# Performance work log

Measured on AMD Instinct MI355X. Metric: run time of the kernel, lower is better.

## Reference

```python
import jax, jax.numpy as jnp
import numpy as np
from functools import partial
from jax import lax

B, K, CLIP_DIM, SBERT_DIM, D_MODEL, R_RANK, ATTN_DIM, PMAX = 128, 1024, 768, 384, 256, 64, 256, 8
RHO = 0.35

def _normalize(x, axis=-1, eps=1e-12):
    return x / jnp.maximum(jnp.linalg.norm(x, axis=axis, keepdims=True), eps)

def _build_graph():
    rng = np.random.default_rng(0)
    pid = np.zeros((K, PMAX), np.int32)
    pm = np.zeros((K, PMAX), bool)
    for i in range(K - 1):  # node i's parents are in (i, K); root = K-1 has none
        n = int(rng.integers(1, PMAX + 1))
        n = min(n, K - 1 - i)
        cands = rng.choice(np.arange(i + 1, K), size=n, replace=False)
        pid[i, :n] = cands
        pm[i, :n] = True
    order = np.arange(K - 1, -1, -1, dtype=np.int32)  # parents before children
    return jnp.asarray(pid), jnp.asarray(pm), jnp.asarray(order)

def setup_inputs() -> dict:
    key = jax.random.key(0)
    ks = iter(jax.random.split(key, 32))
    r = lambda shape, s=0.02: jax.random.normal(next(ks), shape, jnp.float32) * s
    pid, pm, order = _build_graph()
    return {
        "t_clip": jax.random.normal(next(ks), (B, CLIP_DIM), jnp.float32),
        "v_clip": jax.random.normal(next(ks), (B, CLIP_DIM), jnp.float32),
        "concept_sbert": jax.random.normal(next(ks), (K, SBERT_DIM), jnp.float32),
        "Wt": r((CLIP_DIM, D_MODEL)), "bt": jnp.zeros((D_MODEL,)),
        "Wv": r((CLIP_DIM, D_MODEL)), "bv": jnp.zeros((D_MODEL,)),
        "Wc": r((SBERT_DIM, D_MODEL)), "bc": jnp.zeros((D_MODEL,)),
        "Wp1": r((3 * D_MODEL, 2 * D_MODEL)), "bp1": jnp.zeros((2 * D_MODEL,)),
        "Wp2": r((2 * D_MODEL, D_MODEL)), "bp2": jnp.zeros((D_MODEL,)),
        "Wm1": r((3 * D_MODEL, 2 * D_MODEL)), "bm1": jnp.zeros((2 * D_MODEL,)),
        "Wm2": r((2 * D_MODEL, D_MODEL)), "bm2": jnp.zeros((D_MODEL,)),
        "tau_logits": jnp.zeros((K,)),
        "U": r((D_MODEL, R_RANK)), "V": r((D_MODEL, R_RANK)),
        "Wg1": r((SBERT_DIM, R_RANK)), "bg1": jnp.zeros((R_RANK,)),
        "Wg2": r((R_RANK, R_RANK)), "bg2": jnp.zeros((R_RANK,)),
        "w_out": r((K, R_RANK)), "b_out": jnp.zeros((K,)),
        "concept_q": r((K, ATTN_DIM)),
        "parents_idx": pid, "parents_mask": pm, "order": order,
    }

def _forward(t_clip, v_clip, concept_sbert, Wt, bt, Wv, bv, Wc, bc,
             Wp1, bp1, Wp2, bp2, Wm1, bm1, Wm2, bm2, tau_logits,
             U, V, Wg1, bg1, Wg2, bg2, w_out, b_out, concept_q,
             parents_idx, parents_mask, order):
    gelu = partial(jax.nn.gelu, approximate=False)  # torch nn.GELU default = exact erf
    t = _normalize(t_clip) @ Wt + bt                 # [B, D]
    v = _normalize(v_clip) @ Wv + bv                 # [B, D]
    d = concept_sbert @ Wc + bc                      # [K, D]
    # x = [v, t, d] broadcast to [B, K, 3D]
    x = jnp.concatenate([
        jnp.broadcast_to(v[:, None, :], (t.shape[0], K, D_MODEL)),
        jnp.broadcast_to(t[:, None, :], (t.shape[0], K, D_MODEL)),
        jnp.broadcast_to(d[None, :, :], (t.shape[0], K, D_MODEL)),
    ], axis=-1)
    h_plus = gelu(x @ Wp1 + bp1) @ Wp2 + bp2
    h_minus = gelu(x @ Wm1 + bm1) @ Wm2 + bm2
    tau = jax.nn.sigmoid(tau_logits)[None, :, None]
    h = tau * h_plus + (1.0 - tau) * h_minus         # [B, K, D]
    u = jnp.einsum('bkd,dr->bkr', h, U)
    vv = jnp.einsum('bkd,dr->bkr', h, V)
    g = gelu(concept_sbert @ Wg1 + bg1) @ Wg2 + bg2  # [K, R]
    inter = u * vv * g[None, :, :]
    logits = jnp.einsum('bkr,kr->bk', inter, w_out) + b_out[None, :]
    p = jax.nn.sigmoid(logits)                        # [B, K]
    # --- top-down hierarchical attention + multiplicative aggregation ---
    q = _normalize(concept_q)                         # [K, A]
    def step(p_hat, node):
        par = parents_idx[node]                       # [P] int
        m = parents_mask[node]                        # [P] bool
        scores = jnp.where(m, q[par] @ q[node], -1e9)
        alpha = jax.nn.softmax(scores)                # [P]
        vals = p_hat[:, par]                          # [B, P] gather of parent probs
        prod = jnp.prod(jnp.where(m[None, :], alpha[None, :] * vals, 1.0), axis=-1)
        new = jnp.where(m.any(), RHO * p[:, node] + (1.0 - RHO) * prod, p_hat[:, node])
        return p_hat.at[:, node].set(new), None       # scatter write
    p_hat, _ = lax.scan(step, p, order)
    return p_hat

def reference(t_clip, v_clip, concept_sbert, Wt, bt, Wv, bv, Wc, bc,
              Wp1, bp1, Wp2, bp2, Wm1, bm1, Wm2, bm2, tau_logits,
              U, V, Wg1, bg1, Wg2, bg2, w_out, b_out, concept_q,
              parents_idx, parents_mask, order):
    return _forward(t_clip, v_clip, concept_sbert, Wt, bt, Wv, bv, Wc, bc,
                    Wp1, bp1, Wp2, bp2, Wm1, bm1, Wm2, bm2, tau_logits,
                    U, V, Wg1, bg1, Wg2, bg2, w_out, b_out, concept_q,
                    parents_idx, parents_mask, order)
```

## Files before the change

kernel.cpp:

```cpp
#include <hip/hip_runtime.h>
#include <math.h>

typedef __attribute__((ext_vector_type(8))) short short8;
typedef __attribute__((ext_vector_type(4))) float float4v;
typedef __attribute__((ext_vector_type(2))) float float2v;

struct P {
  const float *t_clip, *v_clip, *sbert;
  const float *Wt, *bt, *Wv, *bv, *Wc, *bc;
  const float *Wp1, *bp1, *Wp2, *bp2, *Wm1, *bm1, *Wm2, *bm2;
  const float *tau_logits, *U, *V, *Wg1, *bg1, *Wg2, *bg2, *w_out, *b_out, *concept_q;
  const int *pid;
  float *Ap, *Am;
  unsigned short *Ctp, *Ctm;
  unsigned short *Wpk, *Wmk;
  float *biasPM, *tau, *gw, *aprod;
  unsigned short *parS;
  int *sorted, *lvlStart, *nlev;
  float *pOut;
};

__device__ __forceinline__ unsigned short bf16ru(float f) {
    unsigned u = __float_as_uint(f);
    u += 0x7fffu + ((u >> 16) & 1u);
    return (unsigned short)(u >> 16);
}

__device__ __forceinline__ unsigned packpair(float2v a, unsigned c) {
    float2v cb;
    cb.x = __uint_as_float(c << 16);
    cb.y = __uint_as_float(c & 0xffff0000u);
    float2v x = a + cb;
    float2v t = x * x;
    float2v i = t * (-0.06649038f) + 0.39894228f;
    float2v p = x * i + 0.5f;
    float2v g = x * p;
    union { float2v f; unsigned u[2]; } gu; gu.f = g;
    return __builtin_amdgcn_perm(gu.u[1], gu.u[0], 0x07060302u);
}


__device__ void ab_f(const P& a, int b, float* smemF) {
    float* raw = smemF;
    float* vt  = smemF + 1536;
    float* red = smemF + 2060;
    int t = threadIdx.x;
    float sT = 0.f, sV = 0.f;
    for (int i = t; i < 768; i += 256) {
        float xt = a.t_clip[(size_t)b * 768 + i];
        float xv = a.v_clip[(size_t)b * 768 + i];
        raw[i] = xt; raw[768 + i] = xv;
        sT = fmaf(xt, xt, sT); sV = fmaf(xv, xv, sV);
    }
    for (int mk = 32; mk; mk >>= 1) { sT += __shfl_xor(sT, mk); sV += __shfl_xor(sV, mk); }
    if ((t & 63) == 0) { red[t >> 6] = sT; red[4 + (t >> 6)] = sV; }
    __syncthreads();
    float scT = 1.0f / fmaxf(sqrtf(red[0] + red[1] + red[2] + red[3]), 1e-12f);
    float scV = 1.0f / fmaxf(sqrtf(red[4] + red[5] + red[6] + red[7]), 1e-12f);
    float accT = 0.f, accV = 0.f;
    for (int d = 0; d < 768; ++d) {
        accT = fmaf(raw[d],       a.Wt[(size_t)d * 256 + t], accT);
        accV = fmaf(raw[768 + d], a.Wv[(size_t)d * 256 + t], accV);
    }
    vt[t]       = accV * scV + a.bv[t];
    vt[256 + t] = accT * scT + a.bt[t];
    __syncthreads();
    int mat = t >> 7, j0 = (t & 127) * 4;
    const float* W1 = mat ? a.Wm1 : a.Wp1;
    const float* b1 = mat ? a.bm1 : a.bp1;
    float* out = mat ? a.Am : a.Ap;
    float a0 = 0, a1 = 0, a2 = 0, a3 = 0;
    for (int d = 0; d < 512; ++d) {
        float4 w = *(const float4*)&W1[(size_t)d * 512 + j0];
        float x = vt[d];
        a0 = fmaf(x, w.x, a0); a1 = fmaf(x, w.y, a1);
        a2 = fmaf(x, w.z, a2); a3 = fmaf(x, w.w, a3);
    }
    float4 bb = *(const float4*)&b1[j0];
    float4 o; o.x = a0 + bb.x; o.y = a1 + bb.y; o.z = a2 + bb.z; o.w = a3 + bb.w;
    *(float4*)&out[(size_t)b * 512 + j0] = o;
}

__device__ void c_f(const P& a, int blk, float* smemF) {
    int k0 = blk * 2;
    float* sb = smemF;
    float* dr = smemF + 768;
    int t = threadIdx.x;
    for (int i = t; i < 768; i += 256) sb[i] = a.sbert[(size_t)k0 * 384 + i];
    __syncthreads();
    float d0 = 0.f, d1 = 0.f;
    for (int dd = 0; dd < 384; ++dd) {
        float w = a.Wc[(size_t)dd * 256 + t];
        d0 = fmaf(sb[dd], w, d0);
        d1 = fmaf(sb[384 + dd], w, d1);
    }
    dr[t] = d0 + a.bc[t];
    dr[256 + t] = d1 + a.bc[t];
    __syncthreads();
    int mat = t >> 7, j0 = (t & 127) * 4;
    const float* W1 = mat ? a.Wm1 : a.Wp1;
    unsigned short* out = mat ? a.Ctm : a.Ctp;
    float a00 = 0, a01 = 0, a02 = 0, a03 = 0, a10 = 0, a11 = 0, a12 = 0, a13 = 0;
    for (int dd = 0; dd < 256; ++dd) {
        float4 w = *(const float4*)&W1[(size_t)(512 + dd) * 512 + j0];
        float x0 = dr[dd], x1 = dr[256 + dd];
        a00 = fmaf(x0, w.x, a00); a01 = fmaf(x0, w.y, a01);
        a02 = fmaf(x0, w.z, a02); a03 = fmaf(x0, w.w, a03);
        a10 = fmaf(x1, w.x, a10); a11 = fmaf(x1, w.y, a11);
        a12 = fmaf(x1, w.z, a12); a13 = fmaf(x1, w.w, a13);
    }
    int step = j0 >> 5, quad = (j0 >> 3) & 3, e0 = j0 & 7;
#pragma unroll
    for (int r = 0; r < 2; ++r) {
        int k = k0 + r;
        size_t idx = (size_t)(k >> 4) * 8192 + step * 512 + quad * 128 + (k & 15) * 8 + e0;
        ushort4 o;
        o.x = bf16ru(r ? a10 : a00); o.y = bf16ru(r ? a11 : a01);
        o.z = bf16ru(r ? a12 : a02); o.w = bf16ru(r ? a13 : a03);
        *(ushort4*)&out[idx] = o;
    }
}

__device__ void packW_f(const float* __restrict__ W2, const float* __restrict__ U,
                        const float* __restrict__ V, unsigned short* __restrict__ outP, int rel) {
    int idx = rel * 256 + threadIdx.x;
    int j = idx >> 7, c = idx & 127;
    const float* uv = (c < 64) ? (U + c) : (V + (c - 64));
    float acc = 0.f;
    for (int d = 0; d < 256; ++d) acc = fmaf(W2[(size_t)j * 256 + d], uv[(size_t)d * 64], acc);
    size_t o = (size_t)(j >> 5) * 4096 + (c >> 4) * 512 + ((j >> 3) & 3) * 128 + (c & 15) * 8 + (j & 7);
    outP[o] = bf16ru(acc);
}

__device__ void gw_f(const P& a, int blk, float* ghid) {
    int t = threadIdx.x, wv = t >> 6, lane = t & 63;
    int k = blk * 4 + wv;
    float acc = a.bg1[lane];
    for (int d = 0; d < 384; ++d)
        acc = fmaf(a.sbert[(size_t)k * 384 + d], a.Wg1[(size_t)d * 64 + lane], acc);
    ghid[wv * 64 + lane] = 0.5f * acc * (1.0f + erff(acc * 0.7071067811865475f));
    __syncthreads();
    float acc2 = a.bg2[lane];
    for (int d = 0; d < 64; ++d)
        acc2 = fmaf(ghid[wv * 64 + d], a.Wg2[(size_t)d * 64 + lane], acc2);
    a.gw[(size_t)k * 64 + lane] = acc2 * a.w_out[(size_t)k * 64 + lane];
}

__device__ void alpha_f(const P& a, int blk) {
    int t = threadIdx.x, wv = t >> 6, lane = t & 63;
    int node = blk * 4 + wv;
    int slot = lane >> 3, e = lane & 7;
    int par = a.pid[node * 8 + slot];
    const float4* qk = (const float4*)(a.concept_q + (size_t)node * 256);
    const float4* qp = (const float4*)(a.concept_q + (size_t)par * 256);
    float dq = 0, np = 0, ns = 0;
#pragma unroll
    for (int i = 0; i < 8; ++i) {
        float4 x = qp[e * 8 + i], y = qk[e * 8 + i];
        dq += x.x * y.x + x.y * y.y + x.z * y.z + x.w * y.w;
        np += x.x * x.x + x.y * x.y + x.z * x.z + x.w * x.w;
        ns += y.x * y.x + y.y * y.y + y.z * y.z + y.w * y.w;
    }
#pragma unroll
    for (int mk = 1; mk <= 4; mk <<= 1) {
        dq += __shfl_xor(dq, mk); np += __shfl_xor(np, mk); ns += __shfl_xor(ns, mk);
    }
    float score = dq / fmaxf(sqrtf(np) * sqrtf(ns), 1e-24f);
    float sc[8]; int pv[8];
#pragma unroll
    for (int s = 0; s < 8; ++s) { sc[s] = __shfl(score, s * 8); pv[s] = __shfl(par, s * 8); }
    float mx = -1e30f;
#pragma unroll
    for (int s = 0; s < 8; ++s) if (pv[s] != 0) mx = fmaxf(mx, sc[s]);
    float sum = 0.f;
#pragma unroll
    for (int s = 0; s < 8; ++s) sum += (pv[s] != 0) ? expf(sc[s] - mx) : 0.0f;
    float ap = 1.0f;
#pragma unroll
    for (int s = 0; s < 8; ++s) if (pv[s] != 0) ap *= expf(sc[s] - mx) / sum;
    if (lane == 0) a.aprod[node] = ap;
    if (e == 0) a.parS[node * 8 + slot] = (par != 0) ? (unsigned short)par : (unsigned short)1024;
}

__device__ void misc_f(const P& a, int g) {
    int t = threadIdx.x;
    if (g == 0) {
        int c = t & 127;
        const float* bb = (t < 128) ? a.bp2 : a.bm2;
        const float* uv = (c < 64) ? (a.U + c) : (a.V + (c - 64));
        float acc = 0.f;
        for (int d = 0; d < 256; ++d) acc = fmaf(bb[d], uv[(size_t)d * 64], acc);
        a.biasPM[t] = acc;
    } else {
        int k = (g - 1) * 256 + t;
        a.tau[k] = 1.0f / (1.0f + expf(-a.tau_logits[k]));
    }
}

__device__ void levels_f(const P& a, int* smemI) {
    volatile int* lvl = smemI;
    int* cnt  = smemI + 1024;
    int* ofs  = smemI + 2048;
    int* ping = smemI + 3072;
    int* pong = smemI + 3328;
    int* mflag = smemI + 3584;
    int t = threadIdx.x;
    int par[4][8]; int hasm[4];
#pragma unroll
    for (int r = 0; r < 4; ++r) {
        int n = t * 4 + r, h = 0;
#pragma unroll
        for (int s = 0; s < 8; ++s) { int p = a.pid[n * 8 + s]; par[r][s] = p; h |= (p != 0); }
        hasm[r] = h; lvl[n] = 0;
    }
    if (t == 0) mflag[1] = 0;
    __syncthreads();
    for (int round = 0; round < 200; ++round) {
        if (t == 0) mflag[0] = 0;
        __syncthreads();
        int ch = 0;
        for (int sub = 0; sub < 8; ++sub) {
#pragma unroll
            for (int r = 0; r < 4; ++r) {
                if (!hasm[r]) continue;
                int mx = 0;
#pragma unroll
                for (int s = 0; s < 8; ++s) { int p = par[r][s]; if (p) mx = max(mx, lvl[p]); }
                int nl = mx + 1;
                if (nl > lvl[t * 4 + r]) { lvl[t * 4 + r] = nl; ch = 1; }
            }
        }
        if (ch) mflag[0] = 1;
        __syncthreads();
        if (mflag[0] == 0) break;
    }
    int lm = 0;
    for (int r = 0; r < 4; ++r) lm = max(lm, lvl[t * 4 + r]);
    atomicMax(&mflag[1], lm);
    for (int r = 0; r < 4; ++r) cnt[t * 4 + r] = 0;
    __syncthreads();
    for (int r = 0; r < 4; ++r) atomicAdd(&cnt[lvl[t * 4 + r]], 1);
    __syncthreads();
    int c0 = cnt[t * 4], c1 = cnt[t * 4 + 1], c2 = cnt[t * 4 + 2], c3 = cnt[t * 4 + 3];
    ping[t] = c0 + c1 + c2 + c3;
    __syncthreads();
    int* src = ping; int* dst = pong;
    for (int off = 1; off < 256; off <<= 1) {
        int v = src[t];
        if (t >= off) v += src[t - off];
        dst[t] = v;
        __syncthreads();
        int* tmp = src; src = dst; dst = tmp;
    }
    int excl = (t == 0) ? 0 : src[t - 1];
    ofs[t * 4] = excl; ofs[t * 4 + 1] = excl + c0;
    ofs[t * 4 + 2] = excl + c0 + c1; ofs[t * 4 + 3] = excl + c0 + c1 + c2;
#pragma unroll
    for (int r = 0; r < 4; ++r) a.lvlStart[t * 4 + r] = ofs[t * 4 + r];
    if (t == 0) { a.lvlStart[1024] = 1024; a.nlev[0] = mflag[1] + 1; }
    __syncthreads();
    for (int r = 0; r < 4; ++r) {
        int n = t * 4 + r;
        int pos = atomicAdd(&ofs[lvl[n]], 1);
        a.sorted[pos] = n;
    }
}

__global__ void __launch_bounds__(256) prep_kernel(P a) {
    __shared__ float smemF[4096];
    int bid = blockIdx.x;
    if (bid == 0) { levels_f(a, (int*)smemF); return; }
    bid -= 1;
    if (bid < 128) { ab_f(a, bid, smemF); return; }
    bid -= 128;
    if (bid < 512) { c_f(a, bid, smemF); return; }
    bid -= 512;
    if (bid < 256) { packW_f(a.Wp2, a.U, a.V, a.Wpk, bid); return; }
    bid -= 256;
    if (bid < 256) { packW_f(a.Wm2, a.U, a.V, a.Wmk, bid); return; }
    bid -= 256;
    if (bid < 256) { gw_f(a, bid, smemF); return; }
    bid -= 256;
    if (bid < 256) { alpha_f(a, bid); return; }
    bid -= 256;
    misc_f(a, bid);
}

__global__ void __launch_bounds__(256, 2) main_kernel(P a) {
    __shared__ float apL[4 * 512];
    __shared__ char wbuf[2][16384];
    int tid = threadIdx.x;
    int wv = tid >> 6, lane = tid & 63;
    int b0 = (blockIdx.x >> 4) * 2;
    int k0 = (blockIdx.x & 15) << 6;
    int m = lane & 15, quad = lane >> 4;

    for (int i = tid; i < 512; i += 256) {
        int arr = i >> 7, off = i & 127;
        const float* src = (arr == 0) ? (a.Ap + (size_t)b0 * 512)
                         : (arr == 1) ? (a.Ap + (size_t)(b0 + 1) * 512)
                         : (arr == 2) ? (a.Am + (size_t)b0 * 512)
                                      : (a.Am + (size_t)(b0 + 1) * 512);
        ((float4v*)apL)[i] = ((const float4v*)src)[off];
    }

    const char* wpG = (const char*)a.Wpk;
    const char* wmG = (const char*)a.Wmk;
    int so = tid * 16;
    uint4 wreg[4];
#define LOADW(step) do { \
    wreg[0] = *(const uint4*)(wpG + (size_t)(step) * 8192 + so); \
    wreg[1] = *(const uint4*)(wpG + (size_t)(step) * 8192 + 4096 + so); \
    wreg[2] = *(const uint4*)(wmG + (size_t)(step) * 8192 + so); \
    wreg[3] = *(const uint4*)(wmG + (size_t)(step) * 8192 + 4096 + so); } while (0)
#define WRITEW(buf) do { \
    *(uint4*)(&wbuf[buf][so])         = wreg[0]; \
    *(uint4*)(&wbuf[buf][4096 + so])  = wreg[1]; \
    *(uint4*)(&wbuf[buf][8192 + so])  = wreg[2]; \
    *(uint4*)(&wbuf[buf][12288 + so]) = wreg[3]; } while (0)

    int kt = (k0 >> 4) + wv;
    const char* cpB = (const char*)a.Ctp + (size_t)kt * 16384 + quad * 256 + m * 16;
    const char* cmB = (const char*)a.Ctm + (size_t)kt * 16384 + quad * 256 + m * 16;

    float4v accP[2][8], accM[2][8];
#pragma unroll
    for (int b = 0; b < 2; ++b)
#pragma unroll
        for (int i = 0; i < 8; ++i) { accP[b][i] = (float4v)0.0f; accM[b][i] = (float4v)0.0f; }

    LOADW(0);
    WRITEW(0);
    uint4 cprN = *(const uint4*)(cpB);
    uint4 cmrN = *(const uint4*)(cmB);
    LOADW(1);
    __syncthreads();

    for (int n = 0; n < 16; ++n) {
        if (n < 15) WRITEW((n + 1) & 1);
        if (n < 14) LOADW(n + 2);
        uint4 cprC = cprN, cmrC = cmrN;
        if (n < 15) {
            cprN = *(const uint4*)(cpB + (n + 1) * 1024);
            cmrN = *(const uint4*)(cmB + (n + 1) * 1024);
        }
        const float* aBase = apL + n * 32 + quad * 8;
        union { uint4 u; short8 s; } fp[2], fm[2];
#pragma unroll
        for (int b = 0; b < 2; ++b) {
            float4v x0 = *(const float4v*)(aBase + b * 512);
            float4v x1 = *(const float4v*)(aBase + b * 512 + 4);
            float4v y0 = *(const float4v*)(aBase + (2 + b) * 512);
            float4v y1 = *(const float4v*)(aBase + (2 + b) * 512 + 4);
            float2v v;
            v.x = x0[0]; v.y = x0[1]; fp[b].u.x = packpair(v, cprC.x);
            v.x = x0[2]; v.y = x0[3]; fp[b].u.y = packpair(v, cprC.y);
            v.x = x1[0]; v.y = x1[1]; fp[b].u.z = packpair(v, cprC.z);
            v.x = x1[2]; v.y = x1[3]; fp[b].u.w = packpair(v, cprC.w);
            v.x = y0[0]; v.y = y0[1]; fm[b].u.x = packpair(v, cmrC.x);
            v.x = y0[2]; v.y = y0[3]; fm[b].u.y = packpair(v, cmrC.y);
            v.x = y1[0]; v.y = y1[1]; fm[b].u.z = packpair(v, cmrC.z);
            v.x = y1[2]; v.y = y1[3]; fm[b].u.w = packpair(v, cmrC.w);
        }
        const char* wB = &wbuf[n & 1][0] + quad * 256 + m * 16;
#pragma unroll
        for (int nt = 0; nt < 8; ++nt) {
            short8 wpf = *(const short8*)(wB + nt * 1024);
            short8 wmf = *(const short8*)(wB + 8192 + nt * 1024);
            accP[0][nt] = __builtin_amdgcn_mfma_f32_16x16x32_bf16(fp[0].s, wpf, accP[0][nt], 0, 0, 0);
            accP[1][nt] = __builtin_amdgcn_mfma_f32_16x16x32_bf16(fp[1].s, wpf, accP[1][nt], 0, 0, 0);
            accM[0][nt] = __builtin_amdgcn_mfma_f32_16x16x32_bf16(fm[0].s, wmf, accM[0][nt], 0, 0, 0);
            accM[1][nt] = __builtin_amdgcn_mfma_f32_16x16x32_bf16(fm[1].s, wmf, accM[1][nt], 0, 0, 0);
        }
        __syncthreads();
    }
#undef LOADW
#undef WRITEW
    int kk[4]; float tv[4];
#pragma unroll
    for (int r = 0; r < 4; ++r) { kk[r] = k0 + wv * 16 + quad * 4 + r; tv[r] = a.tau[kk[r]]; }
    float lsum[2][4] = {{0.f,0.f,0.f,0.f},{0.f,0.f,0.f,0.f}};
#pragma unroll
    for (int t4 = 0; t4 < 4; ++t4) {
        int cU = t4 * 16 + m, cV = cU + 64;
        float bPu = a.biasPM[cU], bMu = a.biasPM[128 + cU];
        float bPv = a.biasPM[cV], bMv = a.biasPM[128 + cV];
#pragma unroll
        for (int r = 0; r < 4; ++r) {
            float g = a.gw[(size_t)kk[r] * 64 + cU];
#pragma unroll
            for (int b = 0; b < 2; ++b) {
                float u  = tv[r] * (accP[b][t4][r] + bPu)     + (1.0f - tv[r]) * (accM[b][t4][r] + bMu);
                float vx = tv[r] * (accP[b][t4 + 4][r] + bPv) + (1.0f - tv[r]) * (accM[b][t4 + 4][r] + bMv);
                lsum[b][r] = fmaf(u * vx, g, lsum[b][r]);
            }
        }
    }
#pragma unroll
    for (int r = 0; r < 4; ++r)
#pragma unroll
        for (int b = 0; b < 2; ++b) {
            float s = lsum[b][r];
            s += __shfl_xor(s, 1); s += __shfl_xor(s, 2); s += __shfl_xor(s, 4); s += __shfl_xor(s, 8);
            if (m == 0) {
                float logit = s + a.b_out[kk[r]];
                a.pOut[(size_t)(b0 + b) * 1024 + kk[r]] = 1.0f / (1.0f + expf(-logit));
            }
        }
}

#define PH_STRIDE 1056
__global__ void __launch_bounds__(256) scan_kernel(P a) {
    __shared__ float ph[4 * PH_STRIDE];
    __shared__ float aprodL[1024];
    __shared__ unsigned short parL[8192];
    __shared__ short sortedL[1024];
    __shared__ int lvlStartL[1025];
    int t = threadIdx.x;
    int b0 = blockIdx.x * 4;
    for (int i = t; i < 1024; i += 256) {
        ((uint4*)parL)[i & 1023] = ((const uint4*)a.parS)[i];
    }
    for (int i = t; i < 1024; i += 256) {
        aprodL[i] = a.aprod[i];
        sortedL[i] = (short)a.sorted[i];
        lvlStartL[i] = a.lvlStart[i];
    }
    if (t == 0) lvlStartL[1024] = 1024;
    for (int i = t; i < 4096; i += 256) {
        int bb = i >> 10, k = i & 1023;
        ph[bb * PH_STRIDE + k] = a.pOut[(size_t)(b0 + bb) * 1024 + k];
    }
    if (t < 4) ph[t * PH_STRIDE + 1024] = 1.0f;
    __syncthreads();
    int nlev = a.nlev[0];
    int w = t >> 6, lane = t & 63;
    float* myph = ph + w * PH_STRIDE;
    for (int L = 1; L < nlev; ++L) {
        int s0 = lvlStartL[L], s1 = lvlStartL[L + 1];
        for (int i = s0 + lane; i < s1; i += 64) {
            int node = sortedL[i];
            ushort4 pA = *(const ushort4*)&parL[node * 8];
            ushort4 pB = *(const ushort4*)&parL[node * 8 + 4];
            float prod = aprodL[node];
            prod *= myph[pA.x] * myph[pA.y];
            prod *= myph[pA.z] * myph[pA.w];
            prod *= myph[pB.x] * myph[pB.y];
            prod *= myph[pB.z] * myph[pB.w];
            myph[node] = fmaf(0.35f, myph[node], 0.65f * prod);
        }
    }
    __syncthreads();
    for (int i = t; i < 4096; i += 256) {
        int bb = i >> 10, k = i & 1023;
        a.pOut[(size_t)(b0 + bb) * 1024 + k] = ph[bb * PH_STRIDE + k];
    }
}

extern "C" void kernel_launch(void* const* d_in, const int* in_sizes, int n_in,
                              void* d_out, int out_size, void* d_ws, size_t ws_size,
                              hipStream_t stream) {
    P a;
    a.t_clip = (const float*)d_in[0];
    a.v_clip = (const float*)d_in[1];
    a.sbert  = (const float*)d_in[2];
    a.Wt  = (const float*)d_in[3];  a.bt  = (const float*)d_in[4];
    a.Wv  = (const float*)d_in[5];  a.bv  = (const float*)d_in[6];
    a.Wc  = (const float*)d_in[7];  a.bc  = (const float*)d_in[8];
    a.Wp1 = (const float*)d_in[9];  a.bp1 = (const float*)d_in[10];
    a.Wp2 = (const float*)d_in[11]; a.bp2 = (const float*)d_in[12];
    a.Wm1 = (const float*)d_in[13]; a.bm1 = (const float*)d_in[14];
    a.Wm2 = (const float*)d_in[15]; a.bm2 = (const float*)d_in[16];
    a.tau_logits = (const float*)d_in[17];
    a.U   = (const float*)d_in[18]; a.V   = (const float*)d_in[19];
    a.Wg1 = (const float*)d_in[20]; a.bg1 = (const float*)d_in[21];
    a.Wg2 = (const float*)d_in[22]; a.bg2 = (const float*)d_in[23];
    a.w_out = (const float*)d_in[24]; a.b_out = (const float*)d_in[25];
    a.concept_q = (const float*)d_in[26];
    a.pid = (const int*)d_in[27];

    char* w = (char*)d_ws;
    a.Ap     = (float*)(w + 0);
    a.Am     = (float*)(w + 262144);
    a.Ctp    = (unsigned short*)(w + 524288);
    a.Ctm    = (unsigned short*)(w + 1572864);
    a.Wpk    = (unsigned short*)(w + 2621440);
    a.Wmk    = (unsigned short*)(w + 2752512);
    a.biasPM = (float*)(w + 2883584);
    a.tau    = (float*)(w + 2884608);
    a.gw     = (float*)(w + 2888704);
    a.parS   = (unsigned short*)(w + 3150848);
    a.aprod  = (float*)(w + 3167232);
    a.sorted = (int*)(w + 3171328);
    a.lvlStart = (int*)(w + 3175424);
    a.nlev     = (int*)(w + 3179648);
    a.pOut = (float*)d_out;

    prep_kernel<<<1670, 256, 0, stream>>>(a);
    main_kernel<<<1024, 256, 0, stream>>>(a);
    scan_kernel<<<32, 256, 0, stream>>>(a);
}
```

Measured before the change: 282.6 us.

## Split prep into cache-warming and compute kernels, retile main GEMM per matrix

```diff
diff --git a/kernel.cpp b/kernel.cpp
--- a/kernel.cpp
+++ b/kernel.cpp
@@ -17,6 +17,7 @@
   float *biasPM, *tau, *gw, *aprod;
   unsigned short *parS;
   int *sorted, *lvlStart, *nlev;
+  float *sink;
   float *pOut;
 };
 
@@ -40,85 +41,13 @@
 }
 
 
-__device__ void ab_f(const P& a, int b, float* smemF) {
-    float* raw = smemF;
-    float* vt  = smemF + 1536;
-    float* red = smemF + 2060;
-    int t = threadIdx.x;
-    float sT = 0.f, sV = 0.f;
-    for (int i = t; i < 768; i += 256) {
-        float xt = a.t_clip[(size_t)b * 768 + i];
-        float xv = a.v_clip[(size_t)b * 768 + i];
-        raw[i] = xt; raw[768 + i] = xv;
-        sT = fmaf(xt, xt, sT); sV = fmaf(xv, xv, sV);
-    }
-    for (int mk = 32; mk; mk >>= 1) { sT += __shfl_xor(sT, mk); sV += __shfl_xor(sV, mk); }
-    if ((t & 63) == 0) { red[t >> 6] = sT; red[4 + (t >> 6)] = sV; }
-    __syncthreads();
-    float scT = 1.0f / fmaxf(sqrtf(red[0] + red[1] + red[2] + red[3]), 1e-12f);
-    float scV = 1.0f / fmaxf(sqrtf(red[4] + red[5] + red[6] + red[7]), 1e-12f);
-    float accT = 0.f, accV = 0.f;
-    for (int d = 0; d < 768; ++d) {
-        accT = fmaf(raw[d],       a.Wt[(size_t)d * 256 + t], accT);
-        accV = fmaf(raw[768 + d], a.Wv[(size_t)d * 256 + t], accV);
-    }
-    vt[t]       = accV * scV + a.bv[t];
-    vt[256 + t] = accT * scT + a.bt[t];
-    __syncthreads();
-    int mat = t >> 7, j0 = (t & 127) * 4;
-    const float* W1 = mat ? a.Wm1 : a.Wp1;
-    const float* b1 = mat ? a.bm1 : a.bp1;
-    float* out = mat ? a.Am : a.Ap;
-    float a0 = 0, a1 = 0, a2 = 0, a3 = 0;
-    for (int d = 0; d < 512; ++d) {
-        float4 w = *(const float4*)&W1[(size_t)d * 512 + j0];
-        float x = vt[d];
-        a0 = fmaf(x, w.x, a0); a1 = fmaf(x, w.y, a1);
-        a2 = fmaf(x, w.z, a2); a3 = fmaf(x, w.w, a3);
-    }
-    float4 bb = *(const float4*)&b1[j0];
-    float4 o; o.x = a0 + bb.x; o.y = a1 + bb.y; o.z = a2 + bb.z; o.w = a3 + bb.w;
-    *(float4*)&out[(size_t)b * 512 + j0] = o;
-}
-
-__device__ void c_f(const P& a, int blk, float* smemF) {
-    int k0 = blk * 2;
-    float* sb = smemF;
-    float* dr = smemF + 768;
-    int t = threadIdx.x;
-    for (int i = t; i < 768; i += 256) sb[i] = a.sbert[(size_t)k0 * 384 + i];
-    __syncthreads();
-    float d0 = 0.f, d1 = 0.f;
-    for (int dd = 0; dd < 384; ++dd) {
-        float w = a.Wc[(size_t)dd * 256 + t];
-        d0 = fmaf(sb[dd], w, d0);
-        d1 = fmaf(sb[384 + dd], w, d1);
-    }
-    dr[t] = d0 + a.bc[t];
-    dr[256 + t] = d1 + a.bc[t];
-    __syncthreads();
-    int mat = t >> 7, j0 = (t & 127) * 4;
-    const float* W1 = mat ? a.Wm1 : a.Wp1;
-    unsigned short* out = mat ? a.Ctm : a.Ctp;
-    float a00 = 0, a01 = 0, a02 = 0, a03 = 0, a10 = 0, a11 = 0, a12 = 0, a13 = 0;
-    for (int dd = 0; dd < 256; ++dd) {
-        float4 w = *(const float4*)&W1[(size_t)(512 + dd) * 512 + j0];
-        float x0 = dr[dd], x1 = dr[256 + dd];
-        a00 = fmaf(x0, w.x, a00); a01 = fmaf(x0, w.y, a01);
-        a02 = fmaf(x0, w.z, a02); a03 = fmaf(x0, w.w, a03);
-        a10 = fmaf(x1, w.x, a10); a11 = fmaf(x1, w.y, a11);
-        a12 = fmaf(x1, w.z, a12); a13 = fmaf(x1, w.w, a13);
-    }
-    int step = j0 >> 5, quad = (j0 >> 3) & 3, e0 = j0 & 7;
-#pragma unroll
-    for (int r = 0; r < 2; ++r) {
-        int k = k0 + r;
-        size_t idx = (size_t)(k >> 4) * 8192 + step * 512 + quad * 128 + (k & 15) * 8 + e0;
-        ushort4 o;
-        o.x = bf16ru(r ? a10 : a00); o.y = bf16ru(r ? a11 : a01);
-        o.z = bf16ru(r ? a12 : a02); o.w = bf16ru(r ? a13 : a03);
-        *(ushort4*)&out[idx] = o;
-    }
+__device__ void warm_f(const float* p, int n4, int blk, float* sink) {
+    float4 s = {0.f, 0.f, 0.f, 0.f};
+    for (int i = blk * 1024 + threadIdx.x; i < n4; i += 1024) {
+        float4 v = ((const float4*)p)[i];
+        s.x += v.x; s.y += v.y; s.z += v.z; s.w += v.w;
+    }
+    if (s.x + s.y + s.z + s.w == 1.234567e37f) *sink = s.x;
 }
 
 __device__ void packW_f(const float* __restrict__ W2, const float* __restrict__ U,
@@ -130,56 +59,6 @@
     for (int d = 0; d < 256; ++d) acc = fmaf(W2[(size_t)j * 256 + d], uv[(size_t)d * 64], acc);
     size_t o = (size_t)(j >> 5) * 4096 + (c >> 4) * 512 + ((j >> 3) & 3) * 128 + (c & 15) * 8 + (j & 7);
     outP[o] = bf16ru(acc);
-}
-
-__device__ void gw_f(const P& a, int blk, float* ghid) {
-    int t = threadIdx.x, wv = t >> 6, lane = t & 63;
-    int k = blk * 4 + wv;
-    float acc = a.bg1[lane];
-    for (int d = 0; d < 384; ++d)
-        acc = fmaf(a.sbert[(size_t)k * 384 + d], a.Wg1[(size_t)d * 64 + lane], acc);
-    ghid[wv * 64 + lane] = 0.5f * acc * (1.0f + erff(acc * 0.7071067811865475f));
-    __syncthreads();
-    float acc2 = a.bg2[lane];
-    for (int d = 0; d < 64; ++d)
-        acc2 = fmaf(ghid[wv * 64 + d], a.Wg2[(size_t)d * 64 + lane], acc2);
-    a.gw[(size_t)k * 64 + lane] = acc2 * a.w_out[(size_t)k * 64 + lane];
-}
-
-__device__ void alpha_f(const P& a, int blk) {
-    int t = threadIdx.x, wv = t >> 6, lane = t & 63;
-    int node = blk * 4 + wv;
-    int slot = lane >> 3, e = lane & 7;
-    int par = a.pid[node * 8 + slot];
-    const float4* qk = (const float4*)(a.concept_q + (size_t)node * 256);
-    const float4* qp = (const float4*)(a.concept_q + (size_t)par * 256);
-    float dq = 0, np = 0, ns = 0;
-#pragma unroll
-    for (int i = 0; i < 8; ++i) {
-        float4 x = qp[e * 8 + i], y = qk[e * 8 + i];
-        dq += x.x * y.x + x.y * y.y + x.z * y.z + x.w * y.w;
-        np += x.x * x.x + x.y * x.y + x.z * x.z + x.w * x.w;
-        ns += y.x * y.x + y.y * y.y + y.z * y.z + y.w * y.w;
-    }
-#pragma unroll
-    for (int mk = 1; mk <= 4; mk <<= 1) {
-        dq += __shfl_xor(dq, mk); np += __shfl_xor(np, mk); ns += __shfl_xor(ns, mk);
-    }
-    float score = dq / fmaxf(sqrtf(np) * sqrtf(ns), 1e-24f);
-    float sc[8]; int pv[8];
-#pragma unroll
-    for (int s = 0; s < 8; ++s) { sc[s] = __shfl(score, s * 8); pv[s] = __shfl(par, s * 8); }
-    float mx = -1e30f;
-#pragma unroll
-    for (int s = 0; s < 8; ++s) if (pv[s] != 0) mx = fmaxf(mx, sc[s]);
-    float sum = 0.f;
-#pragma unroll
-    for (int s = 0; s < 8; ++s) sum += (pv[s] != 0) ? expf(sc[s] - mx) : 0.0f;
-    float ap = 1.0f;
-#pragma unroll
-    for (int s = 0; s < 8; ++s) if (pv[s] != 0) ap *= expf(sc[s] - mx) / sum;
-    if (lane == 0) a.aprod[node] = ap;
-    if (e == 0) a.parS[node * 8 + slot] = (par != 0) ? (unsigned short)par : (unsigned short)1024;
 }
 
 __device__ void misc_f(const P& a, int g) {
@@ -266,147 +145,291 @@
     }
 }
 
-__global__ void __launch_bounds__(256) prep_kernel(P a) {
-    __shared__ float smemF[4096];
+__global__ void __launch_bounds__(256) k0_kernel(P a) {
+    __shared__ int smemI[3600];
     int bid = blockIdx.x;
-    if (bid == 0) { levels_f(a, (int*)smemF); return; }
+    if (bid == 0) { levels_f(a, smemI); return; }
     bid -= 1;
-    if (bid < 128) { ab_f(a, bid, smemF); return; }
-    bid -= 128;
-    if (bid < 512) { c_f(a, bid, smemF); return; }
-    bid -= 512;
     if (bid < 256) { packW_f(a.Wp2, a.U, a.V, a.Wpk, bid); return; }
     bid -= 256;
     if (bid < 256) { packW_f(a.Wm2, a.U, a.V, a.Wmk, bid); return; }
     bid -= 256;
+    if (bid < 5) { misc_f(a, bid); return; }
+    bid -= 5;
+    if (bid < 96) { warm_f(a.Wp1, 98304, bid, a.sink); return; }
+    bid -= 96;
+    if (bid < 96) { warm_f(a.Wm1, 98304, bid, a.sink); return; }
+    bid -= 96;
+    if (bid < 48) { warm_f(a.Wt, 49152, bid, a.sink); return; }
+    bid -= 48;
+    if (bid < 48) { warm_f(a.Wv, 49152, bid, a.sink); return; }
+    bid -= 48;
+    if (bid < 24) { warm_f(a.Wc, 24576, bid, a.sink); return; }
+    bid -= 24;
+    if (bid < 96) { warm_f(a.sbert, 98304, bid, a.sink); return; }
+    bid -= 96;
+    if (bid < 24) { warm_f(a.t_clip, 24576, bid, a.sink); return; }
+    bid -= 24;
+    if (bid < 24) { warm_f(a.v_clip, 24576, bid, a.sink); return; }
+    bid -= 24;
+    if (bid < 64) { warm_f(a.concept_q, 65536, bid, a.sink); return; }
+    bid -= 64;
+    if (bid < 16) { warm_f(a.w_out, 16384, bid, a.sink); return; }
+    bid -= 16;
+    warm_f(a.Wg1, 6144, bid, a.sink);
+}
+
+
+__device__ void ab_f(const P& a, int b, float* smemF) {
+    float* raw = smemF;
+    float* vt  = smemF + 1536;
+    float* red = smemF + 2060;
+    int t = threadIdx.x;
+    float sT = 0.f, sV = 0.f;
+    for (int i = t; i < 768; i += 256) {
+        float xt = a.t_clip[(size_t)b * 768 + i];
+        float xv = a.v_clip[(size_t)b * 768 + i];
+        raw[i] = xt; raw[768 + i] = xv;
+        sT = fmaf(xt, xt, sT); sV = fmaf(xv, xv, sV);
+    }
+    for (int mk = 32; mk; mk >>= 1) { sT += __shfl_xor(sT, mk); sV += __shfl_xor(sV, mk); }
+    if ((t & 63) == 0) { red[t >> 6] = sT; red[4 + (t >> 6)] = sV; }
+    __syncthreads();
+    float scT = 1.0f / fmaxf(sqrtf(red[0] + red[1] + red[2] + red[3]), 1e-12f);
+    float scV = 1.0f / fmaxf(sqrtf(red[4] + red[5] + red[6] + red[7]), 1e-12f);
+    float accT = 0.f, accV = 0.f;
+    for (int d = 0; d < 768; ++d) {
+        accT = fmaf(raw[d],       a.Wt[(size_t)d * 256 + t], accT);
+        accV = fmaf(raw[768 + d], a.Wv[(size_t)d * 256 + t], accV);
+    }
+    vt[t]       = accV * scV + a.bv[t];
+    vt[256 + t] = accT * scT + a.bt[t];
+    __syncthreads();
+    int mat = t >> 7, j0 = (t & 127) * 4;
+    const float* W1 = mat ? a.Wm1 : a.Wp1;
+    const float* b1 = mat ? a.bm1 : a.bp1;
+    float* out = mat ? a.Am : a.Ap;
+    float a0 = 0, a1 = 0, a2 = 0, a3 = 0;
+    for (int d = 0; d < 512; ++d) {
+        float4 w = *(const float4*)&W1[(size_t)d * 512 + j0];
+        float x = vt[d];
+        a0 = fmaf(x, w.x, a0); a1 = fmaf(x, w.y, a1);
+        a2 = fmaf(x, w.z, a2); a3 = fmaf(x, w.w, a3);
+    }
+    float4 bb = *(const float4*)&b1[j0];
+    float4 o; o.x = a0 + bb.x; o.y = a1 + bb.y; o.z = a2 + bb.z; o.w = a3 + bb.w;
+    *(float4*)&out[(size_t)b * 512 + j0] = o;
+}
+
+__device__ void c_f(const P& a, int blk, float* smemF) {
+    int k0 = blk * 4;
+    float* sb = smemF;
+    float* dr = smemF + 1536;
+    int t = threadIdx.x;
+    for (int i = t; i < 1536; i += 256) sb[i] = a.sbert[(size_t)k0 * 384 + i];
+    __syncthreads();
+    float d0 = 0, d1 = 0, d2 = 0, d3 = 0;
+    for (int dd = 0; dd < 384; ++dd) {
+        float w = a.Wc[(size_t)dd * 256 + t];
+        d0 = fmaf(sb[dd], w, d0);
+        d1 = fmaf(sb[384 + dd], w, d1);
+        d2 = fmaf(sb[768 + dd], w, d2);
+        d3 = fmaf(sb[1152 + dd], w, d3);
+    }
+    float bcv = a.bc[t];
+    dr[t] = d0 + bcv; dr[256 + t] = d1 + bcv; dr[512 + t] = d2 + bcv; dr[768 + t] = d3 + bcv;
+    __syncthreads();
+    int mat = t >> 7, j0 = (t & 127) * 4;
+    const float* W1 = mat ? a.Wm1 : a.Wp1;
+    unsigned short* out = mat ? a.Ctm : a.Ctp;
+    float acc[4][4] = {};
+    for (int dd = 0; dd < 256; ++dd) {
+        float4 w = *(const float4*)&W1[(size_t)(512 + dd) * 512 + j0];
+#pragma unroll
+        for (int r = 0; r < 4; ++r) {
+            float x = dr[r * 256 + dd];
+            acc[r][0] = fmaf(x, w.x, acc[r][0]); acc[r][1] = fmaf(x, w.y, acc[r][1]);
+            acc[r][2] = fmaf(x, w.z, acc[r][2]); acc[r][3] = fmaf(x, w.w, acc[r][3]);
+        }
+    }
+    int step = j0 >> 5, quad = (j0 >> 3) & 3, e0 = j0 & 7;
+#pragma unroll
+    for (int r = 0; r < 4; ++r) {
+        int k = k0 + r;
+        size_t idx = (size_t)(k >> 4) * 8192 + step * 512 + quad * 128 + (k & 15) * 8 + e0;
+        ushort4 o;
+        o.x = bf16ru(acc[r][0]); o.y = bf16ru(acc[r][1]);
+        o.z = bf16ru(acc[r][2]); o.w = bf16ru(acc[r][3]);
+        *(ushort4*)&out[idx] = o;
+    }
+}
+
+__device__ void gw_f(const P& a, int blk, float* ghid) {
+    int t = threadIdx.x, wv = t >> 6, lane = t & 63;
+    int k = blk * 4 + wv;
+    float acc = a.bg1[lane];
+    for (int d = 0; d < 384; ++d)
+        acc = fmaf(a.sbert[(size_t)k * 384 + d], a.Wg1[(size_t)d * 64 + lane], acc);
+    ghid[wv * 64 + lane] = 0.5f * acc * (1.0f + erff(acc * 0.7071067811865475f));
+    __syncthreads();
+    float acc2 = a.bg2[lane];
+    for (int d = 0; d < 64; ++d)
+        acc2 = fmaf(ghid[wv * 64 + d], a.Wg2[(size_t)d * 64 + lane], acc2);
+    a.gw[(size_t)k * 64 + lane] = acc2 * a.w_out[(size_t)k * 64 + lane];
+}
+
+__device__ void alpha_f(const P& a, int blk) {
+    int t = threadIdx.x, wv = t >> 6, lane = t & 63;
+    int node = blk * 4 + wv;
+    int slot = lane >> 3, e = lane & 7;
+    int par = a.pid[node * 8 + slot];
+    const float4* qk = (const float4*)(a.concept_q + (size_t)node * 256);
+    const float4* qp = (const float4*)(a.concept_q + (size_t)par * 256);
+    float dq = 0, np = 0, ns = 0;
+#pragma unroll
+    for (int i = 0; i < 8; ++i) {
+        float4 x = qp[e * 8 + i], y = qk[e * 8 + i];
+        dq += x.x * y.x + x.y * y.y + x.z * y.z + x.w * y.w;
+        np += x.x * x.x + x.y * x.y + x.z * x.z + x.w * x.w;
+        ns += y.x * y.x + y.y * y.y + y.z * y.z + y.w * y.w;
+    }
+#pragma unroll
+    for (int mk = 1; mk <= 4; mk <<= 1) {
+        dq += __shfl_xor(dq, mk); np += __shfl_xor(np, mk); ns += __shfl_xor(ns, mk);
+    }
+    float score = dq / fmaxf(sqrtf(np) * sqrtf(ns), 1e-24f);
+    float sc[8]; int pv[8];
+#pragma unroll
+    for (int s = 0; s < 8; ++s) { sc[s] = __shfl(score, s * 8); pv[s] = __shfl(par, s * 8); }
+    float mx = -1e30f;
+#pragma unroll
+    for (int s = 0; s < 8; ++s) if (pv[s] != 0) mx = fmaxf(mx, sc[s]);
+    float sum = 0.f;
+#pragma unroll
+    for (int s = 0; s < 8; ++s) sum += (pv[s] != 0) ? expf(sc[s] - mx) : 0.0f;
+    float ap = 1.0f;
+#pragma unroll
+    for (int s = 0; s < 8; ++s) if (pv[s] != 0) ap *= expf(sc[s] - mx) / sum;
+    if (lane == 0) a.aprod[node] = ap;
+    if (e == 0) a.parS[node * 8 + slot] = (par != 0) ? (unsigned short)par : (unsigned short)1024;
+}
+
+__global__ void __launch_bounds__(256) k1_kernel(P a) {
+    __shared__ float smemF[2600];
+    int bid = blockIdx.x;
+    if (bid < 128) { ab_f(a, bid, smemF); return; }
+    bid -= 128;
+    if (bid < 256) { c_f(a, bid, smemF); return; }
+    bid -= 256;
     if (bid < 256) { gw_f(a, bid, smemF); return; }
     bid -= 256;
-    if (bid < 256) { alpha_f(a, bid); return; }
-    bid -= 256;
-    misc_f(a, bid);
-}
-
-__global__ void __launch_bounds__(256, 2) main_kernel(P a) {
-    __shared__ float apL[4 * 512];
-    __shared__ char wbuf[2][16384];
+    alpha_f(a, bid);
+}
+
+__global__ void __launch_bounds__(512, 2) main_kernel(P a) {
+    __shared__ float apL[4096];
+    __shared__ float xbuf[4 * 4 * 64 * 8];
     int tid = threadIdx.x;
-    int wv = tid >> 6, lane = tid & 63;
-    int b0 = (blockIdx.x >> 4) * 2;
+    int wv2 = tid >> 6, lane = tid & 63;
+    int mat = wv2 >> 2, sub = wv2 & 3;
+    int m = lane & 15, quad = lane >> 4;
+    int b0 = (blockIdx.x >> 4) * 4;
     int k0 = (blockIdx.x & 15) << 6;
-    int m = lane & 15, quad = lane >> 4;
-
-    for (int i = tid; i < 512; i += 256) {
+
+    for (int i = tid; i < 1024; i += 512) {
         int arr = i >> 7, off = i & 127;
-        const float* src = (arr == 0) ? (a.Ap + (size_t)b0 * 512)
-                         : (arr == 1) ? (a.Ap + (size_t)(b0 + 1) * 512)
-                         : (arr == 2) ? (a.Am + (size_t)b0 * 512)
-                                      : (a.Am + (size_t)(b0 + 1) * 512);
-        ((float4v*)apL)[i] = ((const float4v*)src)[off];
-    }
-
-    const char* wpG = (const char*)a.Wpk;
-    const char* wmG = (const char*)a.Wmk;
-    int so = tid * 16;
-    uint4 wreg[4];
-#define LOADW(step) do { \
-    wreg[0] = *(const uint4*)(wpG + (size_t)(step) * 8192 + so); \
-    wreg[1] = *(const uint4*)(wpG + (size_t)(step) * 8192 + 4096 + so); \
-    wreg[2] = *(const uint4*)(wmG + (size_t)(step) * 8192 + so); \
-    wreg[3] = *(const uint4*)(wmG + (size_t)(step) * 8192 + 4096 + so); } while (0)
-#define WRITEW(buf) do { \
-    *(uint4*)(&wbuf[buf][so])         = wreg[0]; \
-    *(uint4*)(&wbuf[buf][4096 + so])  = wreg[1]; \
-    *(uint4*)(&wbuf[buf][8192 + so])  = wreg[2]; \
-    *(uint4*)(&wbuf[buf][12288 + so]) = wreg[3]; } while (0)
-
-    int kt = (k0 >> 4) + wv;
-    const char* cpB = (const char*)a.Ctp + (size_t)kt * 16384 + quad * 256 + m * 16;
-    const char* cmB = (const char*)a.Ctm + (size_t)kt * 16384 + quad * 256 + m * 16;
-
-    float4v accP[2][8], accM[2][8];
-#pragma unroll
-    for (int b = 0; b < 2; ++b)
-#pragma unroll
-        for (int i = 0; i < 8; ++i) { accP[b][i] = (float4v)0.0f; accM[b][i] = (float4v)0.0f; }
-
-    LOADW(0);
-    WRITEW(0);
-    uint4 cprN = *(const uint4*)(cpB);
-    uint4 cmrN = *(const uint4*)(cmB);
-    LOADW(1);
-    __syncthreads();
-
+        const float* src = ((arr >> 2) ? a.Am : a.Ap) + (size_t)(b0 + (arr & 3)) * 512;
+        ((float4*)apL)[i] = ((const float4*)src)[off];
+    }
+    __syncthreads();
+
+    const unsigned short* W  = mat ? a.Wmk : a.Wpk;
+    const unsigned short* Ct = mat ? a.Ctm : a.Ctp;
+    const float* aL = apL + mat * 2048;
+    int kt = (k0 >> 4) + sub;
+    const char* ctB = (const char*)Ct + (size_t)kt * 16384 + quad * 256 + m * 16;
+    const char* wB  = (const char*)W + quad * 256 + m * 16;
+
+    float4v acc[4][8];
+#pragma unroll
+    for (int b = 0; b < 4; ++b)
+#pragma unroll
+        for (int i = 0; i < 8; ++i) acc[b][i] = (float4v)0.0f;
+
+    uint4 crN = *(const uint4*)(ctB);
     for (int n = 0; n < 16; ++n) {
-        if (n < 15) WRITEW((n + 1) & 1);
-        if (n < 14) LOADW(n + 2);
-        uint4 cprC = cprN, cmrC = cmrN;
-        if (n < 15) {
-            cprN = *(const uint4*)(cpB + (n + 1) * 1024);
-            cmrN = *(const uint4*)(cmB + (n + 1) * 1024);
-        }
-        const float* aBase = apL + n * 32 + quad * 8;
-        union { uint4 u; short8 s; } fp[2], fm[2];
-#pragma unroll
-        for (int b = 0; b < 2; ++b) {
-            float4v x0 = *(const float4v*)(aBase + b * 512);
-            float4v x1 = *(const float4v*)(aBase + b * 512 + 4);
-            float4v y0 = *(const float4v*)(aBase + (2 + b) * 512);
-            float4v y1 = *(const float4v*)(aBase + (2 + b) * 512 + 4);
+        uint4 cr = crN;
+        if (n < 15) crN = *(const uint4*)(ctB + (n + 1) * 1024);
+        union { uint4 u; short8 s; } fa[4];
+        const float* aj = aL + n * 32 + quad * 8;
+#pragma unroll
+        for (int b = 0; b < 4; ++b) {
+            float4v x0 = *(const float4v*)(aj + b * 512);
+            float4v x1 = *(const float4v*)(aj + b * 512 + 4);
             float2v v;
-            v.x = x0[0]; v.y = x0[1]; fp[b].u.x = packpair(v, cprC.x);
-            v.x = x0[2]; v.y = x0[3]; fp[b].u.y = packpair(v, cprC.y);
-            v.x = x1[0]; v.y = x1[1]; fp[b].u.z = packpair(v, cprC.z);
-            v.x = x1[2]; v.y = x1[3]; fp[b].u.w = packpair(v, cprC.w);
-            v.x = y0[0]; v.y = y0[1]; fm[b].u.x = packpair(v, cmrC.x);
-            v.x = y0[2]; v.y = y0[3]; fm[b].u.y = packpair(v, cmrC.y);
-            v.x = y1[0]; v.y = y1[1]; fm[b].u.z = packpair(v, cmrC.z);
-            v.x = y1[2]; v.y = y1[3]; fm[b].u.w = packpair(v, cmrC.w);
-        }
-        const char* wB = &wbuf[n & 1][0] + quad * 256 + m * 16;
+            v.x = x0[0]; v.y = x0[1]; fa[b].u.x = packpair(v, cr.x);
+            v.x = x0[2]; v.y = x0[3]; fa[b].u.y = packpair(v, cr.y);
+            v.x = x1[0]; v.y = x1[1]; fa[b].u.z = packpair(v, cr.z);
+            v.x = x1[2]; v.y = x1[3]; fa[b].u.w = packpair(v, cr.w);
+        }
+        const char* wn = wB + n * 8192;
 #pragma unroll
         for (int nt = 0; nt < 8; ++nt) {
-            short8 wpf = *(const short8*)(wB + nt * 1024);
-            short8 wmf = *(const short8*)(wB + 8192 + nt * 1024);
-            accP[0][nt] = __builtin_amdgcn_mfma_f32_16x16x32_bf16(fp[0].s, wpf, accP[0][nt], 0, 0, 0);
-            accP[1][nt] = __builtin_amdgcn_mfma_f32_16x16x32_bf16(fp[1].s, wpf, accP[1][nt], 0, 0, 0);
-            accM[0][nt] = __builtin_amdgcn_mfma_f32_16x16x32_bf16(fm[0].s, wmf, accM[0][nt], 0, 0, 0);
-            accM[1][nt] = __builtin_amdgcn_mfma_f32_16x16x32_bf16(fm[1].s, wmf, accM[1][nt], 0, 0, 0);
-        }
+            short8 wf = *(const short8*)(wn + nt * 1024);
+            acc[0][nt] = __builtin_amdgcn_mfma_f32_16x16x32_bf16(fa[0].s, wf, acc[0][nt], 0, 0, 0);
+            acc[1][nt] = __builtin_amdgcn_mfma_f32_16x16x32_bf16(fa[1].s, wf, acc[1][nt], 0, 0, 0);
+            acc[2][nt] = __builtin_amdgcn_mfma_f32_16x16x32_bf16(fa[2].s, wf, acc[2][nt], 0, 0, 0);
+            acc[3][nt] = __builtin_amdgcn_mfma_f32_16x16x32_bf16(fa[3].s, wf, acc[3][nt], 0, 0, 0);
+        }
+    }
+
+    int kk[4]; float tv[4];
+#pragma unroll
+    for (int r = 0; r < 4; ++r) { kk[r] = k0 + sub * 16 + quad * 4 + r; tv[r] = a.tau[kk[r]]; }
+    float lsum[4][4] = {};
+    float* xb = xbuf + ((sub * 4) * 64 + lane) * 8;
+#pragma unroll
+    for (int t4 = 0; t4 < 4; ++t4) {
         __syncthreads();
-    }
-#undef LOADW
-#undef WRITEW
-    int kk[4]; float tv[4];
-#pragma unroll
-    for (int r = 0; r < 4; ++r) { kk[r] = k0 + wv * 16 + quad * 4 + r; tv[r] = a.tau[kk[r]]; }
-    float lsum[2][4] = {{0.f,0.f,0.f,0.f},{0.f,0.f,0.f,0.f}};
-#pragma unroll
-    for (int t4 = 0; t4 < 4; ++t4) {
-        int cU = t4 * 16 + m, cV = cU + 64;
-        float bPu = a.biasPM[cU], bMu = a.biasPM[128 + cU];
-        float bPv = a.biasPM[cV], bMv = a.biasPM[128 + cV];
+        if (mat == 1) {
+#pragma unroll
+            for (int b = 0; b < 4; ++b) {
+                float* d = xb + b * 512;
+#pragma unroll
+                for (int r = 0; r < 4; ++r) { d[r] = acc[b][t4][r]; d[4 + r] = acc[b][t4 + 4][r]; }
+            }
+        }
+        __syncthreads();
+        if (mat == 0) {
+            int cU = t4 * 16 + m, cV = cU + 64;
+            float bPu = a.biasPM[cU], bMu = a.biasPM[128 + cU];
+            float bPv = a.biasPM[cV], bMv = a.biasPM[128 + cV];
+#pragma unroll
+            for (int b = 0; b < 4; ++b) {
+                const float* d = xb + b * 512;
+#pragma unroll
+                for (int r = 0; r < 4; ++r) {
+                    float g = a.gw[(size_t)kk[r] * 64 + cU];
+                    float u  = tv[r] * (acc[b][t4][r] + bPu)     + (1.0f - tv[r]) * (d[r] + bMu);
+                    float vx = tv[r] * (acc[b][t4 + 4][r] + bPv) + (1.0f - tv[r]) * (d[4 + r] + bMv);
+                    lsum[b][r] = fmaf(u * vx, g, lsum[b][r]);
+                }
+            }
+        }
+    }
+    if (mat == 0) {
 #pragma unroll
         for (int r = 0; r < 4; ++r) {
-            float g = a.gw[(size_t)kk[r] * 64 + cU];
-#pragma unroll
-            for (int b = 0; b < 2; ++b) {
-                float u  = tv[r] * (accP[b][t4][r] + bPu)     + (1.0f - tv[r]) * (accM[b][t4][r] + bMu);
-                float vx = tv[r] * (accP[b][t4 + 4][r] + bPv) + (1.0f - tv[r]) * (accM[b][t4 + 4][r] + bMv);
-                lsum[b][r] = fmaf(u * vx, g, lsum[b][r]);
+            float bo = a.b_out[kk[r]];
+#pragma unroll
+            for (int b = 0; b < 4; ++b) {
+                float s = lsum[b][r];
+                s += __shfl_xor(s, 1); s += __shfl_xor(s, 2); s += __shfl_xor(s, 4); s += __shfl_xor(s, 8);
+                if (m == 0)
+                    a.pOut[(size_t)(b0 + b) * 1024 + kk[r]] = 1.0f / (1.0f + expf(-(s + bo)));
             }
         }
     }
-#pragma unroll
-    for (int r = 0; r < 4; ++r)
-#pragma unroll
-        for (int b = 0; b < 2; ++b) {
-            float s = lsum[b][r];
-            s += __shfl_xor(s, 1); s += __shfl_xor(s, 2); s += __shfl_xor(s, 4); s += __shfl_xor(s, 8);
-            if (m == 0) {
-                float logit = s + a.b_out[kk[r]];
-                a.pOut[(size_t)(b0 + b) * 1024 + kk[r]] = 1.0f / (1.0f + expf(-logit));
-            }
-        }
 }
 
 #define PH_STRIDE 1056
@@ -418,9 +441,7 @@
     __shared__ int lvlStartL[1025];
     int t = threadIdx.x;
     int b0 = blockIdx.x * 4;
-    for (int i = t; i < 1024; i += 256) {
-        ((uint4*)parL)[i & 1023] = ((const uint4*)a.parS)[i];
-    }
+    for (int i = t; i < 1024; i += 256) ((uint4*)parL)[i] = ((const uint4*)a.parS)[i];
     for (int i = t; i < 1024; i += 256) {
         aprodL[i] = a.aprod[i];
         sortedL[i] = (short)a.sorted[i];
@@ -494,9 +515,11 @@
     a.sorted = (int*)(w + 3171328);
     a.lvlStart = (int*)(w + 3175424);
     a.nlev     = (int*)(w + 3179648);
+    a.sink     = (float*)(w + 3179776);
     a.pOut = (float*)d_out;
 
-    prep_kernel<<<1670, 256, 0, stream>>>(a);
-    main_kernel<<<1024, 256, 0, stream>>>(a);
+    k0_kernel<<<1062, 256, 0, stream>>>(a);
+    k1_kernel<<<896, 256, 0, stream>>>(a);
+    main_kernel<<<512, 512, 0, stream>>>(a);
     scan_kernel<<<32, 256, 0, stream>>>(a);
 }
```

Result: slower. 306.8 us (+8.6%).
